# Performance work log

Measured on AMD Instinct MI355X. Metric: run time of the kernel, lower is better.

Reference implementation:

```python
import jax, jax.numpy as jnp
import numpy as np

N_NODES = 100000
N_EDGES = 1600000
DIM = 128


def setup_inputs() -> dict:
    key = jax.random.key(0)
    k1, k2, k3, k4, k5 = jax.random.split(key, 5)
    x = jax.random.normal(k1, (N_NODES, DIM), dtype=jnp.float32)
    edge_index = jax.random.randint(k2, (2, N_EDGES), 0, N_NODES, dtype=jnp.int64)
    s = 1.0 / np.sqrt(DIM)
    W_lin = jax.random.uniform(k3, (DIM, DIM), jnp.float32, -s, s)   # nn.Linear (bias=False)
    W_gcn = jax.random.uniform(k4, (DIM, DIM), jnp.float32, -s, s)   # GCNConv internal lin (bias=False)
    b_gcn = jax.random.uniform(k5, (DIM,), jnp.float32, -s, s)       # GCNConv bias
    return {"x": x, "edge_index": edge_index, "W_lin": W_lin, "W_gcn": W_gcn, "b_gcn": b_gcn}


def reference(x, edge_index, W_lin, W_gcn, b_gcn):
    N = x.shape[0]
    # self.linear (bias=False) then GCNConv's internal linear (bias=False)
    h = (x @ W_lin.T) @ W_gcn.T                                      # [N, D]
    # add self loops (PyG GCNConv default add_self_loops=True)
    loop = jnp.arange(N, dtype=edge_index.dtype)
    row = jnp.concatenate([edge_index[0], loop])                     # source
    col = jnp.concatenate([edge_index[1], loop])                     # target
    # symmetric normalization: deg over targets incl. self loops
    deg = jax.ops.segment_sum(jnp.ones_like(col, dtype=h.dtype), col, num_segments=N)
    dinv = jnp.where(deg > 0, jax.lax.rsqrt(deg), 0.0)               # deg^{-1/2}, inf->0
    norm = dinv[row] * dinv[col]                                     # [E+N]
    # gather -> scale -> scatter-add (aggr='add', flow source_to_target)
    msg = h[row] * norm[:, None]                                     # [E+N, D]
    out = jax.ops.segment_sum(msg, col, num_segments=N) + b_gcn      # [N, D]
    # NOTE: self.relu is `Sequential as ReLU` -> empty Sequential -> identity
    return out
```

## Files before the change

### kernel.cpp

```cpp
#include <hip/hip_runtime.h>
#include <hip/hip_bf16.h>

#define DIM 128
#define NBUCK 1024
#define BCAP 2560

typedef short bf16x8 __attribute__((ext_vector_type(8)));
typedef float f32x4 __attribute__((ext_vector_type(4)));

__device__ __forceinline__ unsigned short f2bf(float f) {
    __hip_bfloat16 h = __float2bfloat16(f);
    return *reinterpret_cast<unsigned short*>(&h);
}
__device__ __forceinline__ float u2f(unsigned int u) {
    union { unsigned int i; float f; } v; v.i = u; return v.f;
}

__global__ __launch_bounds__(256) void partition_kernel(const int* __restrict__ src,
                                                        const int* __restrict__ dst,
                                                        int* __restrict__ bcur,
                                                        unsigned int* __restrict__ ebuf,
                                                        int E, int nchunk) {
    __shared__ int hist[NBUCK];
    __shared__ int base[NBUCK];
    const int t = threadIdx.x;
    for (int i = t; i < NBUCK; i += 256) hist[i] = 0;
    __syncthreads();

    const int e0 = blockIdx.x * nchunk;
    const int e1 = min(e0 + nchunk, E);
    for (int e = e0 + t; e < e1; e += 256)
        atomicAdd(&hist[dst[e] >> 7], 1);
    __syncthreads();

    for (int i = t; i < NBUCK; i += 256) {
        const int c = hist[i];
        base[i] = (c > 0) ? atomicAdd(&bcur[i], c) : 0;
    }
    __syncthreads();

    for (int e = e0 + t; e < e1; e += 256) {
        const int d = dst[e];
        const int b = d >> 7;
        const int pos = atomicAdd(&base[b], 1);
        if (pos < BCAP) {
            const unsigned int p = (unsigned int)src[e] | ((unsigned int)(d & 127) << 17);
            ebuf[(size_t)b * BCAP + pos] = p;
        }
    }
}

__global__ __launch_bounds__(256) void bsort_kernel(const unsigned int* __restrict__ ebuf,
                                                    const int* __restrict__ bcur,
                                                    int* __restrict__ adj,
                                                    int* __restrict__ offs,
                                                    int* __restrict__ degi,
                                                    float* __restrict__ dinv, int N) {
    __shared__ unsigned int ein[BCAP];
    __shared__ int eout[BCAP];
    __shared__ int cnt[128];
    __shared__ int scn[128];
    const int t   = threadIdx.x;
    const int bkt = blockIdx.x;
    const int c   = min(bcur[bkt], BCAP);

    if (t < 128) cnt[t] = 0;
    __syncthreads();
    for (int i = t; i < c; i += 256) {
        const unsigned int p = ebuf[(size_t)bkt * BCAP + i];
        ein[i] = p;
        atomicAdd(&cnt[p >> 17], 1);
    }
    __syncthreads();
    if (t < 128) scn[t] = cnt[t];
    __syncthreads();
    for (int off = 1; off < 128; off <<= 1) {
        int v = (t < 128 && t >= off) ? scn[t - off] : 0;
        __syncthreads();
        if (t < 128) scn[t] += v;
        __syncthreads();
    }
    if (t < 128) {
        const int excl = scn[t] - cnt[t];
        const int node = (bkt << 7) + t;
        if (node < N) {
            offs[node] = bkt * BCAP + excl;
            degi[node] = cnt[t];
            dinv[node] = 1.0f / sqrtf((float)(cnt[t] + 1));
        }
        cnt[t] = excl;
    }
    __syncthreads();
    for (int i = t; i < c; i += 256) {
        const unsigned int p = ein[i];
        const int pos = atomicAdd(&cnt[p >> 17], 1);
        eout[pos] = (int)(p & 0x1FFFF);
    }
    __syncthreads();
    for (int i = t; i < c; i += 256)
        adj[(size_t)bkt * BCAP + i] = eout[i];
}

__global__ __launch_bounds__(128) void wp_kernel(const float* __restrict__ Wg,
                                                 const float* __restrict__ Wl,
                                                 unsigned short* __restrict__ Wpb) {
    int c = blockIdx.x;
    int k = threadIdx.x;
    float s = 0.f;
    for (int j = 0; j < DIM; ++j)
        s = fmaf(Wg[c * DIM + j], Wl[j * DIM + k], s);
    Wpb[c * DIM + k] = f2bf(s);
}

__global__ __launch_bounds__(256) void gemm_mfma_kernel(const float* __restrict__ x,
                                                        const unsigned short* __restrict__ Wpb,
                                                        const float* __restrict__ dinv,
                                                        unsigned short* __restrict__ hbf, int N) {
    __shared__ unsigned short xs[64 * 128];
    __shared__ unsigned short wps[128 * 128];
    const int t = threadIdx.x;
    const int brow = blockIdx.x * 64;

#pragma unroll
    for (int j = 0; j < 8; ++j) {
        const int col = (t >> 4) + j * 16;
        const int kb = t & 15;
        const uint4 v = *(const uint4*)(Wpb + col * 128 + kb * 8);
        *(uint4*)&wps[col * 128 + ((kb ^ (col & 15)) * 8)] = v;
    }
#pragma unroll
    for (int i = 0; i < 4; ++i) {
        const int row = (t >> 4) + i * 16;
        const int kb = t & 15;
        const int g = brow + row;
        float4 a0 = make_float4(0.f, 0.f, 0.f, 0.f), a1 = a0;
        if (g < N) {
            a0 = *(const float4*)(x + (size_t)g * 128 + kb * 8);
            a1 = *(const float4*)(x + (size_t)g * 128 + kb * 8 + 4);
        }
        ushort4 lo, hi;
        lo.x = f2bf(a0.x); lo.y = f2bf(a0.y); lo.z = f2bf(a0.z); lo.w = f2bf(a0.w);
        hi.x = f2bf(a1.x); hi.y = f2bf(a1.y); hi.z = f2bf(a1.z); hi.w = f2bf(a1.w);
        unsigned short* p = &xs[row * 128 + ((kb ^ (row & 15)) * 8)];
        *(ushort4*)p = lo;
        *(ushort4*)(p + 4) = hi;
    }
    __syncthreads();

    const int lane = t & 63, wv = t >> 6;
    const int m16 = lane & 15, quad = lane >> 4;

    f32x4 acc[8];
#pragma unroll
    for (int ct = 0; ct < 8; ++ct) acc[ct] = (f32x4){0.f, 0.f, 0.f, 0.f};

    const int arow = wv * 16 + m16;
#pragma unroll
    for (int s = 0; s < 4; ++s) {
        const int pk = ((s * 4 + quad) ^ m16) * 8;
        const bf16x8 a = *(const bf16x8*)&xs[arow * 128 + pk];
#pragma unroll
        for (int ct = 0; ct < 8; ++ct) {
            const bf16x8 b = *(const bf16x8*)&wps[(ct * 16 + m16) * 128 + pk];
            acc[ct] = __builtin_amdgcn_mfma_f32_16x16x32_bf16(a, b, acc[ct], 0, 0, 0);
        }
    }

    const int r0 = brow + wv * 16 + quad * 4;
    float dv[4];
#pragma unroll
    for (int r = 0; r < 4; ++r) dv[r] = (r0 + r < N) ? dinv[r0 + r] : 0.f;
#pragma unroll
    for (int ct = 0; ct < 8; ++ct) {
        const int col = ct * 16 + m16;
#pragma unroll
        for (int r = 0; r < 4; ++r) {
            if (r0 + r < N)
                hbf[(size_t)(r0 + r) * 128 + col] = f2bf(acc[ct][r] * dv[r]);
        }
    }
}

__global__ __launch_bounds__(256) void gather_kernel(const unsigned short* __restrict__ hbf,
                                                     const int* __restrict__ adj,
                                                     const int* __restrict__ offs,
                                                     const int* __restrict__ degi,
                                                     const float* __restrict__ dinv,
                                                     const float* __restrict__ b,
                                                     float* __restrict__ out, int n) {
    const int wid = (blockIdx.x << 2) + (threadIdx.x >> 6);
    if (wid >= n) return;
    const int lane = threadIdx.x & 63;
    const unsigned int* __restrict__ hb = (const unsigned int*)hbf;

    const unsigned int self = hb[(size_t)wid * 64 + lane];
    float ax = u2f(self << 16);
    float ay = u2f(self & 0xFFFF0000u);

    const int start = offs[wid];
    const int end   = start + degi[wid];
    int j = start;
    for (; j + 4 <= end; j += 4) {
        const int s0 = adj[j + 0];
        const int s1 = adj[j + 1];
        const int s2 = adj[j + 2];
        const int s3 = adj[j + 3];
        const unsigned int v0 = hb[(size_t)s0 * 64 + lane];
        const unsigned int v1 = hb[(size_t)s1 * 64 + lane];
        const unsigned int v2 = hb[(size_t)s2 * 64 + lane];
        const unsigned int v3 = hb[(size_t)s3 * 64 + lane];
        ax += (u2f(v0 << 16) + u2f(v1 << 16)) + (u2f(v2 << 16) + u2f(v3 << 16));
        ay += (u2f(v0 & 0xFFFF0000u) + u2f(v1 & 0xFFFF0000u)) + (u2f(v2 & 0xFFFF0000u) + u2f(v3 & 0xFFFF0000u));
    }
    for (; j < end; ++j) {
        const unsigned int v = hb[(size_t)adj[j] * 64 + lane];
        ax += u2f(v << 16);
        ay += u2f(v & 0xFFFF0000u);
    }
    const float dv = dinv[wid];
    const float2 bb = ((const float2*)b)[lane];
    float2 o;
    o.x = dv * ax + bb.x;
    o.y = dv * ay + bb.y;
    ((float2*)out)[(size_t)wid * 64 + lane] = o;
}

extern "C" void kernel_launch(void* const* d_in, const int* in_sizes, int n_in,
                              void* d_out, int out_size, void* d_ws, size_t ws_size,
                              hipStream_t stream) {
    const float* x  = (const float*)d_in[0];
    const int*   ei = (const int*)d_in[1];
    const float* Wl = (const float*)d_in[2];
    const float* Wg = (const float*)d_in[3];
    const float* bg = (const float*)d_in[4];

    const int N = in_sizes[0] / DIM;
    const int E = in_sizes[1] / 2;
    const int* srcIdx = ei;
    const int* dstIdx = ei + E;

    char* wsb = (char*)d_ws;
    unsigned short* Wpb  = (unsigned short*)(wsb + 0);
    float*          dinv = (float*)(wsb + 65536);
    int*            degi = (int*)  (wsb + 465536);
    int*            offs = (int*)  (wsb + 865536);
    int*            bcur = (int*)  (wsb + 1265536);
    unsigned int*   ebuf = (unsigned int*)(wsb + 2097152);
    int*            adj  = (int*)  (wsb + 12582912);
    unsigned short* hbf  = (unsigned short*)(wsb + 23068672);
    const size_t needed = 23068672ull + (size_t)N * DIM * 2;
    if (ws_size < needed) return;

    hipMemsetAsync(bcur, 0, NBUCK * sizeof(int), stream);

    const int nbkt = (N + 127) >> 7;
    const int nchunk = (E + 255) / 256;

    wp_kernel       <<<DIM, DIM, 0, stream>>>(Wg, Wl, Wpb);
    partition_kernel<<<256, 256, 0, stream>>>(srcIdx, dstIdx, bcur, ebuf, E, nchunk);
    bsort_kernel    <<<nbkt, 256, 0, stream>>>(ebuf, bcur, adj, offs, degi, dinv, N);
    gemm_mfma_kernel<<<(N + 63) / 64, 256, 0, stream>>>(x, Wpb, dinv, hbf, N);
    gather_kernel   <<<(N + 3) / 4, 256, 0, stream>>>(hbf, adj, offs, degi, dinv, bg,
                                                      (float*)d_out, N);
}
```

Before: 241.7 us.

## Merge edge partition and GEMM into one launch, move dinv scaling to gather

The edge-bucketing partition and the bf16 MFMA GEMM now run as two block ranges of one kernel, so the GEMM no longer waits for the partition and sort steps. Because the GEMM runs before dinv exists, the source-side dinv scaling moves into the gather, which now loads dinv[src] for each edge. The bcur memset is folded into wp_kernel, dropping one launch. h is stored with each 32-bit word holding columns c and c+64, so the gather writes output as two coalesced float planes. The cost is an extra dependent scalar load per edge in the gather, which is the main memory-bound stage.

```diff
diff --git a/kernel.cpp b/kernel.cpp
--- a/kernel.cpp
+++ b/kernel.cpp
@@ -16,36 +16,119 @@
     union { unsigned int i; float f; } v; v.i = u; return v.f;
 }
 
-__global__ __launch_bounds__(256) void partition_kernel(const int* __restrict__ src,
-                                                        const int* __restrict__ dst,
-                                                        int* __restrict__ bcur,
-                                                        unsigned int* __restrict__ ebuf,
-                                                        int E, int nchunk) {
-    __shared__ int hist[NBUCK];
-    __shared__ int base[NBUCK];
+__global__ __launch_bounds__(128) void wp_kernel(const float* __restrict__ Wg,
+                                                 const float* __restrict__ Wl,
+                                                 unsigned short* __restrict__ Wpb,
+                                                 int* __restrict__ bcur) {
+    const int c = blockIdx.x;
+    const int k = threadIdx.x;
+    const int gid = c * 128 + k;
+    if (gid < NBUCK) bcur[gid] = 0;
+    float s = 0.f;
+    for (int j = 0; j < DIM; ++j)
+        s = fmaf(Wg[c * DIM + j], Wl[j * DIM + k], s);
+    Wpb[c * DIM + k] = f2bf(s);
+}
+
+__global__ __launch_bounds__(256) void part_gemm_kernel(
+        const int* __restrict__ src, const int* __restrict__ dst,
+        int* __restrict__ bcur, unsigned int* __restrict__ ebuf,
+        int E, int nchunk,
+        const float* __restrict__ x, const unsigned short* __restrict__ Wpb,
+        unsigned int* __restrict__ hbu, int N) {
+    __shared__ __align__(16) char smem[49152];
     const int t = threadIdx.x;
-    for (int i = t; i < NBUCK; i += 256) hist[i] = 0;
-    __syncthreads();
-
-    const int e0 = blockIdx.x * nchunk;
-    const int e1 = min(e0 + nchunk, E);
-    for (int e = e0 + t; e < e1; e += 256)
-        atomicAdd(&hist[dst[e] >> 7], 1);
-    __syncthreads();
-
-    for (int i = t; i < NBUCK; i += 256) {
-        const int c = hist[i];
-        base[i] = (c > 0) ? atomicAdd(&bcur[i], c) : 0;
-    }
-    __syncthreads();
-
-    for (int e = e0 + t; e < e1; e += 256) {
-        const int d = dst[e];
-        const int b = d >> 7;
-        const int pos = atomicAdd(&base[b], 1);
-        if (pos < BCAP) {
-            const unsigned int p = (unsigned int)src[e] | ((unsigned int)(d & 127) << 17);
-            ebuf[(size_t)b * BCAP + pos] = p;
+
+    if (blockIdx.x < 256) {
+        int* hist = (int*)smem;
+        int* base = hist + NBUCK;
+        for (int i = t; i < NBUCK; i += 256) hist[i] = 0;
+        __syncthreads();
+
+        const int e0 = blockIdx.x * nchunk;
+        const int e1 = min(e0 + nchunk, E);
+        for (int e = e0 + t; e < e1; e += 256)
+            atomicAdd(&hist[dst[e] >> 7], 1);
+        __syncthreads();
+
+        for (int i = t; i < NBUCK; i += 256) {
+            const int cc = hist[i];
+            base[i] = (cc > 0) ? atomicAdd(&bcur[i], cc) : 0;
+        }
+        __syncthreads();
+
+        for (int e = e0 + t; e < e1; e += 256) {
+            const int d = dst[e];
+            const int b = d >> 7;
+            const int pos = atomicAdd(&base[b], 1);
+            if (pos < BCAP) {
+                const unsigned int p = (unsigned int)src[e] | ((unsigned int)(d & 127) << 17);
+                ebuf[(size_t)b * BCAP + pos] = p;
+            }
+        }
+        return;
+    }
+
+    unsigned short* xs  = (unsigned short*)smem;
+    unsigned short* wps = xs + 64 * 128;
+    const int brow = (blockIdx.x - 256) * 64;
+
+#pragma unroll
+    for (int j = 0; j < 8; ++j) {
+        const int col = (t >> 4) + j * 16;
+        const int kb = t & 15;
+        const uint4 v = *(const uint4*)(Wpb + col * 128 + kb * 8);
+        *(uint4*)&wps[col * 128 + ((kb ^ (col & 15)) * 8)] = v;
+    }
+#pragma unroll
+    for (int i = 0; i < 4; ++i) {
+        const int row = (t >> 4) + i * 16;
+        const int kb = t & 15;
+        const int g = brow + row;
+        float4 a0 = make_float4(0.f, 0.f, 0.f, 0.f), a1 = a0;
+        if (g < N) {
+            a0 = *(const float4*)(x + (size_t)g * 128 + kb * 8);
+            a1 = *(const float4*)(x + (size_t)g * 128 + kb * 8 + 4);
+        }
+        ushort4 lo, hi;
+        lo.x = f2bf(a0.x); lo.y = f2bf(a0.y); lo.z = f2bf(a0.z); lo.w = f2bf(a0.w);
+        hi.x = f2bf(a1.x); hi.y = f2bf(a1.y); hi.z = f2bf(a1.z); hi.w = f2bf(a1.w);
+        unsigned short* p = &xs[row * 128 + ((kb ^ (row & 15)) * 8)];
+        *(ushort4*)p = lo;
+        *(ushort4*)(p + 4) = hi;
+    }
+    __syncthreads();
+
+    const int lane = t & 63, wv = t >> 6;
+    const int m16 = lane & 15, quad = lane >> 4;
+
+    f32x4 acc[8];
+#pragma unroll
+    for (int ct = 0; ct < 8; ++ct) acc[ct] = (f32x4){0.f, 0.f, 0.f, 0.f};
+
+    const int arow = wv * 16 + m16;
+#pragma unroll
+    for (int s = 0; s < 4; ++s) {
+        const int pk = ((s * 4 + quad) ^ m16) * 8;
+        const bf16x8 a = *(const bf16x8*)&xs[arow * 128 + pk];
+#pragma unroll
+        for (int ct = 0; ct < 8; ++ct) {
+            const bf16x8 b = *(const bf16x8*)&wps[(ct * 16 + m16) * 128 + pk];
+            acc[ct] = __builtin_amdgcn_mfma_f32_16x16x32_bf16(a, b, acc[ct], 0, 0, 0);
+        }
+    }
+
+    const int r0 = brow + wv * 16 + quad * 4;
+#pragma unroll
+    for (int ct = 0; ct < 4; ++ct) {
+        const int col = ct * 16 + m16;
+#pragma unroll
+        for (int r = 0; r < 4; ++r) {
+            if (r0 + r < N) {
+                const unsigned int pk = (unsigned int)f2bf(acc[ct][r]) |
+                                        ((unsigned int)f2bf(acc[ct + 4][r]) << 16);
+                hbu[(size_t)(r0 + r) * 64 + col] = pk;
+            }
         }
     }
 }
@@ -101,87 +184,7 @@
         adj[(size_t)bkt * BCAP + i] = eout[i];
 }
 
-__global__ __launch_bounds__(128) void wp_kernel(const float* __restrict__ Wg,
-                                                 const float* __restrict__ Wl,
-                                                 unsigned short* __restrict__ Wpb) {
-    int c = blockIdx.x;
-    int k = threadIdx.x;
-    float s = 0.f;
-    for (int j = 0; j < DIM; ++j)
-        s = fmaf(Wg[c * DIM + j], Wl[j * DIM + k], s);
-    Wpb[c * DIM + k] = f2bf(s);
-}
-
-__global__ __launch_bounds__(256) void gemm_mfma_kernel(const float* __restrict__ x,
-                                                        const unsigned short* __restrict__ Wpb,
-                                                        const float* __restrict__ dinv,
-                                                        unsigned short* __restrict__ hbf, int N) {
-    __shared__ unsigned short xs[64 * 128];
-    __shared__ unsigned short wps[128 * 128];
-    const int t = threadIdx.x;
-    const int brow = blockIdx.x * 64;
-
-#pragma unroll
-    for (int j = 0; j < 8; ++j) {
-        const int col = (t >> 4) + j * 16;
-        const int kb = t & 15;
-        const uint4 v = *(const uint4*)(Wpb + col * 128 + kb * 8);
-        *(uint4*)&wps[col * 128 + ((kb ^ (col & 15)) * 8)] = v;
-    }
-#pragma unroll
-    for (int i = 0; i < 4; ++i) {
-        const int row = (t >> 4) + i * 16;
-        const int kb = t & 15;
-        const int g = brow + row;
-        float4 a0 = make_float4(0.f, 0.f, 0.f, 0.f), a1 = a0;
-        if (g < N) {
-            a0 = *(const float4*)(x + (size_t)g * 128 + kb * 8);
-            a1 = *(const float4*)(x + (size_t)g * 128 + kb * 8 + 4);
-        }
-        ushort4 lo, hi;
-        lo.x = f2bf(a0.x); lo.y = f2bf(a0.y); lo.z = f2bf(a0.z); lo.w = f2bf(a0.w);
-        hi.x = f2bf(a1.x); hi.y = f2bf(a1.y); hi.z = f2bf(a1.z); hi.w = f2bf(a1.w);
-        unsigned short* p = &xs[row * 128 + ((kb ^ (row & 15)) * 8)];
-        *(ushort4*)p = lo;
-        *(ushort4*)(p + 4) = hi;
-    }
-    __syncthreads();
-
-    const int lane = t & 63, wv = t >> 6;
-    const int m16 = lane & 15, quad = lane >> 4;
-
-    f32x4 acc[8];
-#pragma unroll
-    for (int ct = 0; ct < 8; ++ct) acc[ct] = (f32x4){0.f, 0.f, 0.f, 0.f};
-
-    const int arow = wv * 16 + m16;
-#pragma unroll
-    for (int s = 0; s < 4; ++s) {
-        const int pk = ((s * 4 + quad) ^ m16) * 8;
-        const bf16x8 a = *(const bf16x8*)&xs[arow * 128 + pk];
-#pragma unroll
-        for (int ct = 0; ct < 8; ++ct) {
-            const bf16x8 b = *(const bf16x8*)&wps[(ct * 16 + m16) * 128 + pk];
-            acc[ct] = __builtin_amdgcn_mfma_f32_16x16x32_bf16(a, b, acc[ct], 0, 0, 0);
-        }
-    }
-
-    const int r0 = brow + wv * 16 + quad * 4;
-    float dv[4];
-#pragma unroll
-    for (int r = 0; r < 4; ++r) dv[r] = (r0 + r < N) ? dinv[r0 + r] : 0.f;
-#pragma unroll
-    for (int ct = 0; ct < 8; ++ct) {
-        const int col = ct * 16 + m16;
-#pragma unroll
-        for (int r = 0; r < 4; ++r) {
-            if (r0 + r < N)
-                hbf[(size_t)(r0 + r) * 128 + col] = f2bf(acc[ct][r] * dv[r]);
-        }
-    }
-}
-
-__global__ __launch_bounds__(256) void gather_kernel(const unsigned short* __restrict__ hbf,
+__global__ __launch_bounds__(256) void gather_kernel(const unsigned int* __restrict__ hbu,
                                                      const int* __restrict__ adj,
                                                      const int* __restrict__ offs,
                                                      const int* __restrict__ degi,
@@ -191,11 +194,11 @@
     const int wid = (blockIdx.x << 2) + (threadIdx.x >> 6);
     if (wid >= n) return;
     const int lane = threadIdx.x & 63;
-    const unsigned int* __restrict__ hb = (const unsigned int*)hbf;
-
-    const unsigned int self = hb[(size_t)wid * 64 + lane];
-    float ax = u2f(self << 16);
-    float ay = u2f(self & 0xFFFF0000u);
+
+    const float dv = dinv[wid];
+    const unsigned int self = hbu[(size_t)wid * 64 + lane];
+    float ax = dv * u2f(self << 16);
+    float ay = dv * u2f(self & 0xFFFF0000u);
 
     const int start = offs[wid];
     const int end   = start + degi[wid];
@@ -205,24 +208,34 @@
         const int s1 = adj[j + 1];
         const int s2 = adj[j + 2];
         const int s3 = adj[j + 3];
-        const unsigned int v0 = hb[(size_t)s0 * 64 + lane];
-        const unsigned int v1 = hb[(size_t)s1 * 64 + lane];
-        const unsigned int v2 = hb[(size_t)s2 * 64 + lane];
-        const unsigned int v3 = hb[(size_t)s3 * 64 + lane];
-        ax += (u2f(v0 << 16) + u2f(v1 << 16)) + (u2f(v2 << 16) + u2f(v3 << 16));
-        ay += (u2f(v0 & 0xFFFF0000u) + u2f(v1 & 0xFFFF0000u)) + (u2f(v2 & 0xFFFF0000u) + u2f(v3 & 0xFFFF0000u));
+        const float g0 = dinv[s0];
+        const float g1 = dinv[s1];
+        const float g2 = dinv[s2];
+        const float g3 = dinv[s3];
+        const unsigned int v0 = hbu[(size_t)s0 * 64 + lane];
+        const unsigned int v1 = hbu[(size_t)s1 * 64 + lane];
+        const unsigned int v2 = hbu[(size_t)s2 * 64 + lane];
+        const unsigned int v3 = hbu[(size_t)s3 * 64 + lane];
+        ax = fmaf(u2f(v0 << 16), g0, ax);
+        ax = fmaf(u2f(v1 << 16), g1, ax);
+        ax = fmaf(u2f(v2 << 16), g2, ax);
+        ax = fmaf(u2f(v3 << 16), g3, ax);
+        ay = fmaf(u2f(v0 & 0xFFFF0000u), g0, ay);
+        ay = fmaf(u2f(v1 & 0xFFFF0000u), g1, ay);
+        ay = fmaf(u2f(v2 & 0xFFFF0000u), g2, ay);
+        ay = fmaf(u2f(v3 & 0xFFFF0000u), g3, ay);
     }
     for (; j < end; ++j) {
-        const unsigned int v = hb[(size_t)adj[j] * 64 + lane];
-        ax += u2f(v << 16);
-        ay += u2f(v & 0xFFFF0000u);
-    }
-    const float dv = dinv[wid];
-    const float2 bb = ((const float2*)b)[lane];
-    float2 o;
-    o.x = dv * ax + bb.x;
-    o.y = dv * ay + bb.y;
-    ((float2*)out)[(size_t)wid * 64 + lane] = o;
+        const int s = adj[j];
+        const float g = dinv[s];
+        const unsigned int v = hbu[(size_t)s * 64 + lane];
+        ax = fmaf(u2f(v << 16), g, ax);
+        ay = fmaf(u2f(v & 0xFFFF0000u), g, ay);
+    }
+    const float bx = b[lane];
+    const float by = b[lane + 64];
+    out[(size_t)wid * 128 + lane]      = dv * ax + bx;
+    out[(size_t)wid * 128 + 64 + lane] = dv * ay + by;
 }
 
 extern "C" void kernel_launch(void* const* d_in, const int* in_sizes, int n_in,
@@ -241,25 +254,24 @@
 
     char* wsb = (char*)d_ws;
     unsigned short* Wpb  = (unsigned short*)(wsb + 0);
-    float*          dinv = (float*)(wsb + 65536);
-    int*            degi = (int*)  (wsb + 465536);
-    int*            offs = (int*)  (wsb + 865536);
-    int*            bcur = (int*)  (wsb + 1265536);
+    int*            bcur = (int*)(wsb + 65536);
+    float*          dinv = (float*)(wsb + 131072);
+    int*            degi = (int*)(wsb + 531072);
+    int*            offs = (int*)(wsb + 931072);
     unsigned int*   ebuf = (unsigned int*)(wsb + 2097152);
-    int*            adj  = (int*)  (wsb + 12582912);
-    unsigned short* hbf  = (unsigned short*)(wsb + 23068672);
+    int*            adj  = (int*)(wsb + 12582912);
+    unsigned int*   hbu  = (unsigned int*)(wsb + 23068672);
     const size_t needed = 23068672ull + (size_t)N * DIM * 2;
     if (ws_size < needed) return;
 
-    hipMemsetAsync(bcur, 0, NBUCK * sizeof(int), stream);
-
     const int nbkt = (N + 127) >> 7;
+    const int ngemm = (N + 63) / 64;
     const int nchunk = (E + 255) / 256;
 
-    wp_kernel       <<<DIM, DIM, 0, stream>>>(Wg, Wl, Wpb);
-    partition_kernel<<<256, 256, 0, stream>>>(srcIdx, dstIdx, bcur, ebuf, E, nchunk);
+    wp_kernel       <<<DIM, DIM, 0, stream>>>(Wg, Wl, Wpb, bcur);
+    part_gemm_kernel<<<256 + ngemm, 256, 0, stream>>>(srcIdx, dstIdx, bcur, ebuf,
+                                                      E, nchunk, x, Wpb, hbu, N);
     bsort_kernel    <<<nbkt, 256, 0, stream>>>(ebuf, bcur, adj, offs, degi, dinv, N);
-    gemm_mfma_kernel<<<(N + 63) / 64, 256, 0, stream>>>(x, Wpb, dinv, hbf, N);
-    gather_kernel   <<<(N + 3) / 4, 256, 0, stream>>>(hbf, adj, offs, degi, dinv, bg,
+    gather_kernel   <<<(N + 3) / 4, 256, 0, stream>>>(hbu, adj, offs, degi, dinv, bg,
                                                       (float*)d_out, N);
 }
```

Result: faster. 230.5 us (-4.6%).
